# Performance work log

Measured on AMD Instinct MI355X. Metric: run time of the kernel, lower is better.

Reference implementation:

```python
import jax, jax.numpy as jnp
import numpy as np

K_CODES = 512
D_DIM = 64


def setup_inputs() -> dict:
    key = jax.random.key(0)
    k1, k2 = jax.random.split(key)
    # z_e_x: (B, C=D, H, W) encoder output feature map
    z_e_x = jax.random.normal(k1, (32, 64, 64, 64), dtype=jnp.float32)
    # codebook, initialized uniform(-1/K, 1/K) like the torch module
    weight = jax.random.uniform(k2, (K_CODES, D_DIM), dtype=jnp.float32,
                                minval=-1.0 / K_CODES, maxval=1.0 / K_CODES)
    return {"z_e_x": z_e_x, "weight": weight}


def reference(z_e_x, weight):
    # forward(): permute to channels-last, nearest-neighbor codebook lookup,
    # return latent indices of shape (B, H, W)
    z = jnp.transpose(z_e_x, (0, 2, 3, 1))  # (B, H, W, D)
    B, H, W, D = z.shape
    flat = z.reshape(-1, D)  # (N, D)
    # squared L2 distances via expansion: ||z||^2 - 2 z.e + ||e||^2
    dists = (jnp.sum(flat * flat, axis=1, keepdims=True)
             - 2.0 * flat @ weight.T
             + jnp.sum(weight * weight, axis=1))  # (N, K)
    idx = jnp.argmin(dists, axis=1)  # (N,) int
    return idx.reshape(B, H, W)
```

## Files before the change

### kernel.cpp

```cpp
#include <hip/hip_runtime.h>
#include <stdint.h>

#define DCH 64
#define KC 512
#define HWSZ 4096
#define THETA 1e-4f
#define POSB 512
#define BLOCK 1024
#define PADW 65

typedef __attribute__((ext_vector_type(8))) short short8v;
typedef __attribute__((ext_vector_type(4))) float floatx4;

#define WS_WHS   0
#define WS_WLS   65536
#define WS_WNORM 131072
#define WS_CNT   133120
#define WS_LIST  133184
#define WS_NEED  (133184 + 131072 * 4)

__device__ __forceinline__ uint16_t f2bf_rne(float x) {
  uint32_t u = __float_as_uint(x);
  uint32_t r = (u + 0x7fffu + ((u >> 16) & 1u)) >> 16;
  return (uint16_t)r;
}
__device__ __forceinline__ float bf2f(uint16_t b) {
  return __uint_as_float(((uint32_t)b) << 16);
}

__device__ __forceinline__ float pairwise_sq64(const float* __restrict__ a) {
#pragma clang fp contract(off)
  float r0 = a[0]*a[0], r1 = a[1]*a[1], r2 = a[2]*a[2], r3 = a[3]*a[3];
  float r4 = a[4]*a[4], r5 = a[5]*a[5], r6 = a[6]*a[6], r7 = a[7]*a[7];
#pragma unroll
  for (int i = 8; i < 64; i += 8) {
    r0 += a[i+0]*a[i+0]; r1 += a[i+1]*a[i+1];
    r2 += a[i+2]*a[i+2]; r3 += a[i+3]*a[i+3];
    r4 += a[i+4]*a[i+4]; r5 += a[i+5]*a[i+5];
    r6 += a[i+6]*a[i+6]; r7 += a[i+7]*a[i+7];
  }
  return ((r0+r1)+(r2+r3)) + ((r4+r5)+(r6+r7));
}

__device__ __forceinline__ void load_frag(const float* __restrict__ p,
                                          short8v& vh, short8v& vl) {
#pragma unroll
  for (int j = 0; j < 8; ++j) {
    const float v = p[(size_t)j * HWSZ];
    const uint16_t hb = f2bf_rne(v);
    vh[j] = (short)hb;
    vl[j] = (short)f2bf_rne(v - bf2f(hb));
  }
}

__global__ __launch_bounds__(64) void vq_prep(const float* __restrict__ W,
                                              char* __restrict__ ws) {
  const int c = blockIdx.x * 64 + threadIdx.x;
  const float* __restrict__ wr = W + c * DCH;
  float a[64];
#pragma unroll
  for (int i = 0; i < 16; ++i) {
    const float4 v = ((const float4*)wr)[i];
    a[4*i+0] = v.x; a[4*i+1] = v.y; a[4*i+2] = v.z; a[4*i+3] = v.w;
  }
  ((float*)(ws + WS_WNORM))[c] = pairwise_sq64(a);
  uint16_t* wh = (uint16_t*)(ws + WS_WHS);
  uint16_t* wl = (uint16_t*)(ws + WS_WLS);
#pragma unroll
  for (int gd = 0; gd < 8; ++gd) {
    short8v vh, vl;
#pragma unroll
    for (int e = 0; e < 8; ++e) {
      const float v = a[gd * 8 + e];
      const uint16_t hb = f2bf_rne(v);
      vh[e] = (short)hb;
      vl[e] = (short)f2bf_rne(v - bf2f(hb));
    }
    const int go = (gd ^ (c & 7)) << 3;
    *(short8v*)(wh + c * DCH + go) = vh;
    *(short8v*)(wl + c * DCH + go) = vl;
  }
  if (c == 0) *(int*)(ws + WS_CNT) = 0;
}

__global__ __launch_bounds__(BLOCK) void vq_main(const float* __restrict__ Z,
                                                 char* __restrict__ ws,
                                                 int* __restrict__ out) {
  __shared__ uint16_t img[65536];
  __shared__ float wnlds[KC];

  const int tid = threadIdx.x;
  const int lane = tid & 63;
  const int wv = tid >> 6;
  const int csub = lane & 15;
  const int gsub = lane >> 4;
  const int nbase = blockIdx.x * POSB;

  const char* __restrict__ img_src = (const char*)ws;
  const float* __restrict__ wnorm = (const float*)(ws + WS_WNORM);
  int* cnt = (int*)(ws + WS_CNT);
  int* list = (int*)(ws + WS_LIST);

#pragma unroll
  for (int r = 0; r < 8; ++r) {
    const int base = r * 16384 + wv * 1024;
    __builtin_amdgcn_global_load_lds((const uint32_t*)(img_src + base + lane * 16),
                                     (uint32_t*)((char*)img + base), 16, 0, 0);
  }
  if (tid < 128) {
    const int base = wv * 1024;
    __builtin_amdgcn_global_load_lds((const uint32_t*)((const char*)wnorm + base + lane * 16),
                                     (uint32_t*)((char*)wnlds + base), 16, 0, 0);
  }

  short8v ahA0, ahA1, alA0, alA1, ahB0, ahB1, alB0, alB1;
  {
    const int b = nbase >> 12;
    const int hw0 = nbase & 4095;
    const float* zb = Z + (size_t)b * DCH * HWSZ + hw0 + wv * 32 + csub;
    const int dbase = gsub * 8;
    load_frag(zb + (size_t)(dbase +  0) * HWSZ,      ahA0, alA0);
    load_frag(zb + (size_t)(dbase + 32) * HWSZ,      ahA1, alA1);
    load_frag(zb + (size_t)(dbase +  0) * HWSZ + 16, ahB0, alB0);
    load_frag(zb + (size_t)(dbase + 32) * HWSZ + 16, ahB1, alB1);
  }

  float m1A[4], m2A[4], m1B[4], m2B[4];
  int i1A[4], i1B[4];
#pragma unroll
  for (int r = 0; r < 4; ++r) {
    m1A[r] = 3.4e38f; m2A[r] = 3.4e38f; i1A[r] = 0;
    m1B[r] = 3.4e38f; m2B[r] = 3.4e38f; i1B[r] = 0;
  }

  __syncthreads();

  const uint16_t* __restrict__ whl = img;
  const uint16_t* __restrict__ wll = img + 32768;

  const int go0 = (gsub ^ (csub & 7)) << 3;
  const int go1 = ((4 + gsub) ^ (csub & 7)) << 3;

#pragma unroll 8
  for (int kt = 0; kt < KC / 16; ++kt) {
    const int cloc = kt * 16 + csub;
    const float wn = wnlds[cloc];
    const short8v bh0 = *(const short8v*)&whl[cloc * DCH + go0];
    const short8v bh1 = *(const short8v*)&whl[cloc * DCH + go1];
    const short8v bl0 = *(const short8v*)&wll[cloc * DCH + go0];
    const short8v bl1 = *(const short8v*)&wll[cloc * DCH + go1];
    const floatx4 zz = {0.f, 0.f, 0.f, 0.f};
    floatx4 cA1 = __builtin_amdgcn_mfma_f32_16x16x32_bf16(ahA0, bh0, zz, 0, 0, 0);
    floatx4 cB1 = __builtin_amdgcn_mfma_f32_16x16x32_bf16(ahB0, bh0, zz, 0, 0, 0);
    floatx4 cA2 = __builtin_amdgcn_mfma_f32_16x16x32_bf16(ahA0, bl0, zz, 0, 0, 0);
    floatx4 cB2 = __builtin_amdgcn_mfma_f32_16x16x32_bf16(ahB0, bl0, zz, 0, 0, 0);
    floatx4 cA3 = __builtin_amdgcn_mfma_f32_16x16x32_bf16(alA0, bh0, zz, 0, 0, 0);
    floatx4 cB3 = __builtin_amdgcn_mfma_f32_16x16x32_bf16(alB0, bh0, zz, 0, 0, 0);
    cA1 = __builtin_amdgcn_mfma_f32_16x16x32_bf16(ahA1, bh1, cA1, 0, 0, 0);
    cB1 = __builtin_amdgcn_mfma_f32_16x16x32_bf16(ahB1, bh1, cB1, 0, 0, 0);
    cA2 = __builtin_amdgcn_mfma_f32_16x16x32_bf16(ahA1, bl1, cA2, 0, 0, 0);
    cB2 = __builtin_amdgcn_mfma_f32_16x16x32_bf16(ahB1, bl1, cB2, 0, 0, 0);
    cA3 = __builtin_amdgcn_mfma_f32_16x16x32_bf16(alA1, bh1, cA3, 0, 0, 0);
    cB3 = __builtin_amdgcn_mfma_f32_16x16x32_bf16(alB1, bh1, cB3, 0, 0, 0);
#pragma unroll
    for (int r = 0; r < 4; ++r) {
      const float sA = fmaf(-2.0f, (cA1[r] + cA2[r]) + cA3[r], wn);
      i1A[r] = (sA < m1A[r]) ? cloc : i1A[r];
      m2A[r] = fminf(fmaxf(sA, m1A[r]), m2A[r]);
      m1A[r] = fminf(sA, m1A[r]);
      const float sB = fmaf(-2.0f, (cB1[r] + cB2[r]) + cB3[r], wn);
      i1B[r] = (sB < m1B[r]) ? cloc : i1B[r];
      m2B[r] = fminf(fmaxf(sB, m1B[r]), m2B[r]);
      m1B[r] = fminf(sB, m1B[r]);
    }
  }

#pragma unroll
  for (int off = 1; off < 16; off <<= 1) {
#pragma unroll
    for (int r = 0; r < 4; ++r) {
      {
        const float om1 = __shfl_xor(m1A[r], off, 64);
        const float om2 = __shfl_xor(m2A[r], off, 64);
        const int oi = __shfl_xor(i1A[r], off, 64);
        const float nm2 = fminf(fmaxf(m1A[r], om1), fminf(m2A[r], om2));
        i1A[r] = (om1 < m1A[r]) ? oi : i1A[r];
        m1A[r] = fminf(m1A[r], om1);
        m2A[r] = nm2;
      }
      {
        const float om1 = __shfl_xor(m1B[r], off, 64);
        const float om2 = __shfl_xor(m2B[r], off, 64);
        const int oi = __shfl_xor(i1B[r], off, 64);
        const float nm2 = fminf(fmaxf(m1B[r], om1), fminf(m2B[r], om2));
        i1B[r] = (om1 < m1B[r]) ? oi : i1B[r];
        m1B[r] = fminf(m1B[r], om1);
        m2B[r] = nm2;
      }
    }
  }
  if (csub == 0) {
#pragma unroll
    for (int r = 0; r < 4; ++r) {
      const int posA = nbase + wv * 32 + gsub * 4 + r;
      out[posA] = i1A[r];
      if (!(m2A[r] - m1A[r] > THETA)) {
        const int slot = atomicAdd(cnt, 1);
        list[slot] = posA;
      }
      const int posB = posA + 16;
      out[posB] = i1B[r];
      if (!(m2B[r] - m1B[r] > THETA)) {
        const int slot = atomicAdd(cnt, 1);
        list[slot] = posB;
      }
    }
  }
}

__global__ __launch_bounds__(256) void vq_rescue(const float* __restrict__ Z,
                                                 const float* __restrict__ W,
                                                 char* __restrict__ ws,
                                                 int* __restrict__ out) {
  __shared__ float wt[KC * PADW];
  const int cnt = *(const int*)(ws + WS_CNT);
  if (blockIdx.x * 4 >= cnt) return;

  const int lane = threadIdx.x & 63;
  const int wv = threadIdx.x >> 6;
  const int wvg = blockIdx.x * 4 + wv;
  const int* list = (const int*)(ws + WS_LIST);
  const float* wnorm = (const float*)(ws + WS_WNORM);

  for (int c = wv; c < KC; c += 4) {
    wt[c * PADW + lane] = W[c * DCH + lane];
  }
  __syncthreads();

  for (int j = wvg; j < cnt; j += 256 * 4) {
    const int pos = list[j];
    const int b = pos >> 12, hw = pos & 4095;
    float z[DCH];
    const float* zb = Z + ((size_t)b * DCH) * HWSZ + hw;
#pragma unroll
    for (int d = 0; d < DCH; ++d) z[d] = zb[(size_t)d * HWSZ];
    const float znorm = pairwise_sq64(z);
    float bm = 3.4e38f;
    int bi = 0;
#pragma unroll 1
    for (int j2 = 0; j2 < 8; ++j2) {
      const int k = j2 * 64 + lane;
      const float* __restrict__ wrow = &wt[k * PADW];
      float acc = 0.f;
#pragma unroll
      for (int d = 0; d < DCH; ++d) acc = fmaf(z[d], wrow[d], acc);
      const float dist = (znorm - 2.0f * acc) + wnorm[k];
      if (dist < bm) { bm = dist; bi = k; }
    }
#pragma unroll
    for (int off = 32; off >= 1; off >>= 1) {
      const float ov = __shfl_xor(bm, off, 64);
      const int oi = __shfl_xor(bi, off, 64);
      if (ov < bm || (ov == bm && oi < bi)) { bm = ov; bi = oi; }
    }
    if (lane == 0) out[pos] = bi;
  }
}

__global__ __launch_bounds__(256, 4) void vq_fallback(const float* __restrict__ Z,
                                                      const float* __restrict__ W,
                                                      int* __restrict__ out) {
  __shared__ float wnorm[KC];
  __shared__ float cmin[4][64];
  __shared__ int cidx[4][64];
  const int tid = threadIdx.x;
  for (int c = tid; c < KC; c += 256) wnorm[c] = pairwise_sq64(W + c * DCH);
  const int lane = tid & 63;
  const int wv = __builtin_amdgcn_readfirstlane(tid >> 6);
  const int n = blockIdx.x * 64 + lane;
  float z[DCH];
  {
    const int b = n >> 12, hw = n & 4095;
    const float* zbase = Z + ((size_t)b * DCH) * HWSZ + hw;
#pragma unroll
    for (int d = 0; d < DCH; ++d) z[d] = zbase[(size_t)d * HWSZ];
  }
  const float znorm = pairwise_sq64(z);
  __syncthreads();
  float bmin = 3.4e38f;
  int bidx = 0;
  const int k0 = wv * 128;
#pragma unroll 1
  for (int kk = 0; kk < 128; kk += 8) {
    const int k = k0 + kk;
    const float* wr = W + (size_t)k * DCH;
    float acc[8];
#pragma unroll
    for (int j = 0; j < 8; ++j) acc[j] = 0.0f;
#pragma unroll
    for (int d = 0; d < DCH; ++d) {
      const float zd = z[d];
#pragma unroll
      for (int j = 0; j < 8; ++j) acc[j] = fmaf(zd, wr[j * DCH + d], acc[j]);
    }
#pragma unroll
    for (int j = 0; j < 8; ++j) {
      const float dist = (znorm - 2.0f * acc[j]) + wnorm[k + j];
      if (dist < bmin) { bmin = dist; bidx = k + j; }
    }
  }
  cmin[wv][lane] = bmin;
  cidx[wv][lane] = bidx;
  __syncthreads();
  if (tid < 64) {
    float m = cmin[0][tid];
    int ix = cidx[0][tid];
#pragma unroll
    for (int h = 1; h < 4; ++h) {
      if (cmin[h][tid] < m) { m = cmin[h][tid]; ix = cidx[h][tid]; }
    }
    out[blockIdx.x * 64 + tid] = ix;
  }
}

extern "C" void kernel_launch(void* const* d_in, const int* in_sizes, int n_in,
                              void* d_out, int out_size, void* d_ws, size_t ws_size,
                              hipStream_t stream) {
  const float* Z = (const float*)d_in[0];
  const float* W = (const float*)d_in[1];
  int* out = (int*)d_out;
  char* ws = (char*)d_ws;
  const int npos = in_sizes[0] / DCH;

  if (ws_size < (size_t)WS_NEED) {
    vq_fallback<<<npos / 64, 256, 0, stream>>>(Z, W, out);
    return;
  }
  vq_prep<<<8, 64, 0, stream>>>(W, ws);
  vq_main<<<npos / POSB, BLOCK, 0, stream>>>(Z, ws, out);
  vq_rescue<<<256, 256, 0, stream>>>(Z, W, ws, out);
}
```

Measured before the change: 69.71 us.

## Double-buffer codebook staging in LDS and halve positions per block

Each block now handles 256 positions, one 16-row tile per wave instead of two, so the grid has twice as many blocks. The full 128KB codebook image in shared memory is replaced by two 32KB buffers. The codebook is streamed in four quarters, and the next quarter loads while the current one is used by the MFMAs. This cuts the LDS footprint per block, which should allow more blocks per CU and hide the staging latency, at the cost of extra barriers and four times the codebook reloads across the grid.

```diff
diff --git a/kernel.cpp b/kernel.cpp
--- a/kernel.cpp
+++ b/kernel.cpp
@@ -5,7 +5,7 @@
 #define KC 512
 #define HWSZ 4096
 #define THETA 1e-4f
-#define POSB 512
+#define POSB 256
 #define BLOCK 1024
 #define PADW 65
 
@@ -86,7 +86,8 @@
 __global__ __launch_bounds__(BLOCK) void vq_main(const float* __restrict__ Z,
                                                  char* __restrict__ ws,
                                                  int* __restrict__ out) {
-  __shared__ uint16_t img[65536];
+  __shared__ uint16_t buf0[16384];
+  __shared__ uint16_t buf1[16384];
   __shared__ float wnlds[KC];
 
   const int tid = threadIdx.x;
@@ -96,123 +97,100 @@
   const int gsub = lane >> 4;
   const int nbase = blockIdx.x * POSB;
 
-  const char* __restrict__ img_src = (const char*)ws;
+  const char* __restrict__ src_hi = (const char*)ws;
+  const char* __restrict__ src_lo = (const char*)ws + WS_WLS;
   const float* __restrict__ wnorm = (const float*)(ws + WS_WNORM);
   int* cnt = (int*)(ws + WS_CNT);
   int* list = (int*)(ws + WS_LIST);
 
-#pragma unroll
-  for (int r = 0; r < 8; ++r) {
-    const int base = r * 16384 + wv * 1024;
-    __builtin_amdgcn_global_load_lds((const uint32_t*)(img_src + base + lane * 16),
-                                     (uint32_t*)((char*)img + base), 16, 0, 0);
-  }
+  auto STAGE = [&](int q, uint16_t* dst) {
+    const int off = tid * 16;
+    __builtin_amdgcn_global_load_lds((const uint32_t*)(src_hi + q * 16384 + off),
+                                     (uint32_t*)((char*)dst + off), 16, 0, 0);
+    __builtin_amdgcn_global_load_lds((const uint32_t*)(src_lo + q * 16384 + off),
+                                     (uint32_t*)((char*)dst + 16384 + off), 16, 0, 0);
+  };
+
+  STAGE(0, buf0);
   if (tid < 128) {
     const int base = wv * 1024;
     __builtin_amdgcn_global_load_lds((const uint32_t*)((const char*)wnorm + base + lane * 16),
                                      (uint32_t*)((char*)wnlds + base), 16, 0, 0);
   }
 
-  short8v ahA0, ahA1, alA0, alA1, ahB0, ahB1, alB0, alB1;
+  short8v ah0, ah1, al0, al1;
   {
     const int b = nbase >> 12;
     const int hw0 = nbase & 4095;
-    const float* zb = Z + (size_t)b * DCH * HWSZ + hw0 + wv * 32 + csub;
+    const float* zb = Z + (size_t)b * DCH * HWSZ + hw0 + wv * 16 + csub;
     const int dbase = gsub * 8;
-    load_frag(zb + (size_t)(dbase +  0) * HWSZ,      ahA0, alA0);
-    load_frag(zb + (size_t)(dbase + 32) * HWSZ,      ahA1, alA1);
-    load_frag(zb + (size_t)(dbase +  0) * HWSZ + 16, ahB0, alB0);
-    load_frag(zb + (size_t)(dbase + 32) * HWSZ + 16, ahB1, alB1);
-  }
-
-  float m1A[4], m2A[4], m1B[4], m2B[4];
-  int i1A[4], i1B[4];
-#pragma unroll
-  for (int r = 0; r < 4; ++r) {
-    m1A[r] = 3.4e38f; m2A[r] = 3.4e38f; i1A[r] = 0;
-    m1B[r] = 3.4e38f; m2B[r] = 3.4e38f; i1B[r] = 0;
-  }
+    load_frag(zb + (size_t)(dbase +  0) * HWSZ, ah0, al0);
+    load_frag(zb + (size_t)(dbase + 32) * HWSZ, ah1, al1);
+  }
+
+  float m1[4], m2[4];
+  int i1[4];
+#pragma unroll
+  for (int r = 0; r < 4; ++r) { m1[r] = 3.4e38f; m2[r] = 3.4e38f; i1[r] = 0; }
 
   __syncthreads();
-
-  const uint16_t* __restrict__ whl = img;
-  const uint16_t* __restrict__ wll = img + 32768;
 
   const int go0 = (gsub ^ (csub & 7)) << 3;
   const int go1 = ((4 + gsub) ^ (csub & 7)) << 3;
 
-#pragma unroll 8
-  for (int kt = 0; kt < KC / 16; ++kt) {
-    const int cloc = kt * 16 + csub;
-    const float wn = wnlds[cloc];
-    const short8v bh0 = *(const short8v*)&whl[cloc * DCH + go0];
-    const short8v bh1 = *(const short8v*)&whl[cloc * DCH + go1];
-    const short8v bl0 = *(const short8v*)&wll[cloc * DCH + go0];
-    const short8v bl1 = *(const short8v*)&wll[cloc * DCH + go1];
-    const floatx4 zz = {0.f, 0.f, 0.f, 0.f};
-    floatx4 cA1 = __builtin_amdgcn_mfma_f32_16x16x32_bf16(ahA0, bh0, zz, 0, 0, 0);
-    floatx4 cB1 = __builtin_amdgcn_mfma_f32_16x16x32_bf16(ahB0, bh0, zz, 0, 0, 0);
-    floatx4 cA2 = __builtin_amdgcn_mfma_f32_16x16x32_bf16(ahA0, bl0, zz, 0, 0, 0);
-    floatx4 cB2 = __builtin_amdgcn_mfma_f32_16x16x32_bf16(ahB0, bl0, zz, 0, 0, 0);
-    floatx4 cA3 = __builtin_amdgcn_mfma_f32_16x16x32_bf16(alA0, bh0, zz, 0, 0, 0);
-    floatx4 cB3 = __builtin_amdgcn_mfma_f32_16x16x32_bf16(alB0, bh0, zz, 0, 0, 0);
-    cA1 = __builtin_amdgcn_mfma_f32_16x16x32_bf16(ahA1, bh1, cA1, 0, 0, 0);
-    cB1 = __builtin_amdgcn_mfma_f32_16x16x32_bf16(ahB1, bh1, cB1, 0, 0, 0);
-    cA2 = __builtin_amdgcn_mfma_f32_16x16x32_bf16(ahA1, bl1, cA2, 0, 0, 0);
-    cB2 = __builtin_amdgcn_mfma_f32_16x16x32_bf16(ahB1, bl1, cB2, 0, 0, 0);
-    cA3 = __builtin_amdgcn_mfma_f32_16x16x32_bf16(alA1, bh1, cA3, 0, 0, 0);
-    cB3 = __builtin_amdgcn_mfma_f32_16x16x32_bf16(alB1, bh1, cB3, 0, 0, 0);
+#pragma unroll
+  for (int q = 0; q < 4; ++q) {
+    if (q < 3) STAGE(q + 1, (q & 1) ? buf0 : buf1);
+    const uint16_t* __restrict__ bh = (q & 1) ? buf1 : buf0;
+    const uint16_t* __restrict__ bl = bh + 8192;
+#pragma unroll
+    for (int kt = 0; kt < 8; ++kt) {
+      const int cq = kt * 16 + csub;
+      const int cloc = q * 128 + cq;
+      const float wn = wnlds[cloc];
+      const short8v bh0 = *(const short8v*)&bh[cq * DCH + go0];
+      const short8v bh1 = *(const short8v*)&bh[cq * DCH + go1];
+      const short8v bl0 = *(const short8v*)&bl[cq * DCH + go0];
+      const short8v bl1 = *(const short8v*)&bl[cq * DCH + go1];
+      const floatx4 zz = {0.f, 0.f, 0.f, 0.f};
+      floatx4 c1 = __builtin_amdgcn_mfma_f32_16x16x32_bf16(ah0, bh0, zz, 0, 0, 0);
+      floatx4 c2 = __builtin_amdgcn_mfma_f32_16x16x32_bf16(ah0, bl0, zz, 0, 0, 0);
+      floatx4 c3 = __builtin_amdgcn_mfma_f32_16x16x32_bf16(al0, bh0, zz, 0, 0, 0);
+      c1 = __builtin_amdgcn_mfma_f32_16x16x32_bf16(ah1, bh1, c1, 0, 0, 0);
+      c2 = __builtin_amdgcn_mfma_f32_16x16x32_bf16(ah1, bl1, c2, 0, 0, 0);
+      c3 = __builtin_amdgcn_mfma_f32_16x16x32_bf16(al1, bh1, c3, 0, 0, 0);
+#pragma unroll
+      for (int r = 0; r < 4; ++r) {
+        const float s = fmaf(-2.0f, (c1[r] + c2[r]) + c3[r], wn);
+        i1[r] = (s < m1[r]) ? cloc : i1[r];
+        m2[r] = fminf(fmaxf(s, m1[r]), m2[r]);
+        m1[r] = fminf(s, m1[r]);
+      }
+    }
+    if (q < 3) __syncthreads();
+  }
+
+#pragma unroll
+  for (int off = 1; off < 16; off <<= 1) {
 #pragma unroll
     for (int r = 0; r < 4; ++r) {
-      const float sA = fmaf(-2.0f, (cA1[r] + cA2[r]) + cA3[r], wn);
-      i1A[r] = (sA < m1A[r]) ? cloc : i1A[r];
-      m2A[r] = fminf(fmaxf(sA, m1A[r]), m2A[r]);
-      m1A[r] = fminf(sA, m1A[r]);
-      const float sB = fmaf(-2.0f, (cB1[r] + cB2[r]) + cB3[r], wn);
-      i1B[r] = (sB < m1B[r]) ? cloc : i1B[r];
-      m2B[r] = fminf(fmaxf(sB, m1B[r]), m2B[r]);
-      m1B[r] = fminf(sB, m1B[r]);
-    }
-  }
-
-#pragma unroll
-  for (int off = 1; off < 16; off <<= 1) {
+      const float om1 = __shfl_xor(m1[r], off, 64);
+      const float om2 = __shfl_xor(m2[r], off, 64);
+      const int oi = __shfl_xor(i1[r], off, 64);
+      const float nm2 = fminf(fmaxf(m1[r], om1), fminf(m2[r], om2));
+      i1[r] = (om1 < m1[r]) ? oi : i1[r];
+      m1[r] = fminf(m1[r], om1);
+      m2[r] = nm2;
+    }
+  }
+  if (csub == 0) {
 #pragma unroll
     for (int r = 0; r < 4; ++r) {
-      {
-        const float om1 = __shfl_xor(m1A[r], off, 64);
-        const float om2 = __shfl_xor(m2A[r], off, 64);
-        const int oi = __shfl_xor(i1A[r], off, 64);
-        const float nm2 = fminf(fmaxf(m1A[r], om1), fminf(m2A[r], om2));
-        i1A[r] = (om1 < m1A[r]) ? oi : i1A[r];
-        m1A[r] = fminf(m1A[r], om1);
-        m2A[r] = nm2;
-      }
-      {
-        const float om1 = __shfl_xor(m1B[r], off, 64);
-        const float om2 = __shfl_xor(m2B[r], off, 64);
-        const int oi = __shfl_xor(i1B[r], off, 64);
-        const float nm2 = fminf(fmaxf(m1B[r], om1), fminf(m2B[r], om2));
-        i1B[r] = (om1 < m1B[r]) ? oi : i1B[r];
-        m1B[r] = fminf(m1B[r], om1);
-        m2B[r] = nm2;
-      }
-    }
-  }
-  if (csub == 0) {
-#pragma unroll
-    for (int r = 0; r < 4; ++r) {
-      const int posA = nbase + wv * 32 + gsub * 4 + r;
-      out[posA] = i1A[r];
-      if (!(m2A[r] - m1A[r] > THETA)) {
+      const int pos = nbase + wv * 16 + gsub * 4 + r;
+      out[pos] = i1[r];
+      if (!(m2[r] - m1[r] > THETA)) {
         const int slot = atomicAdd(cnt, 1);
-        list[slot] = posA;
-      }
-      const int posB = posA + 16;
-      out[posB] = i1B[r];
-      if (!(m2B[r] - m1B[r] > THETA)) {
-        const int slot = atomicAdd(cnt, 1);
-        list[slot] = posB;
+        list[slot] = pos;
       }
     }
   }
```

New measurement: 85.90 us. 23.2% more time.

## Split codebook across two blocks per position tile and merge partial argmins

Applied to the files above, without the earlier changes.

The main kernel now processes half the codebook (256 codes) per block, launching twice as many blocks, each staging only half the bf16 hi/lo codebook image in LDS. Per-position partial min, second-min and index are written to workspace, and a new combine kernel merges the halves, writes the output and queues ambiguous positions for the existing rescue pass. The intent is more blocks and lower LDS use per block, so occupancy and wave-level parallelism improve on a grid that previously had only 256 blocks. The cost is an extra launch, the Z fragments being loaded and converted twice, and extra global traffic for the partial results. The workspace must also be large enough for the new path to run.

```diff
diff --git a/kernel.cpp b/kernel.cpp
--- a/kernel.cpp
+++ b/kernel.cpp
@@ -3,10 +3,12 @@
 
 #define DCH 64
 #define KC 512
+#define KHALF 256
 #define HWSZ 4096
 #define THETA 1e-4f
 #define POSB 512
 #define BLOCK 1024
+#define NPOS 131072
 #define PADW 65
 
 typedef __attribute__((ext_vector_type(8))) short short8v;
@@ -18,6 +20,10 @@
 #define WS_CNT   133120
 #define WS_LIST  133184
 #define WS_NEED  (133184 + 131072 * 4)
+#define WS_PM1   657472
+#define WS_PM2   (657472 + 1048576)
+#define WS_PI    (657472 + 2097152)
+#define WS_NEED_SPLIT (657472 + 3145728)
 
 __device__ __forceinline__ uint16_t f2bf_rne(float x) {
   uint32_t u = __float_as_uint(x);
@@ -83,34 +89,35 @@
   if (c == 0) *(int*)(ws + WS_CNT) = 0;
 }
 
-__global__ __launch_bounds__(BLOCK) void vq_main(const float* __restrict__ Z,
-                                                 char* __restrict__ ws,
-                                                 int* __restrict__ out) {
-  __shared__ uint16_t img[65536];
-  __shared__ float wnlds[KC];
+__global__ __launch_bounds__(BLOCK) void vq_main_split(const float* __restrict__ Z,
+                                                       char* __restrict__ ws,
+                                                       int npos) {
+  __shared__ uint16_t img[32768];
+  __shared__ float wnlds[KHALF];
 
   const int tid = threadIdx.x;
   const int lane = tid & 63;
   const int wv = tid >> 6;
   const int csub = lane & 15;
   const int gsub = lane >> 4;
-  const int nbase = blockIdx.x * POSB;
-
-  const char* __restrict__ img_src = (const char*)ws;
+  const int h = blockIdx.x & 1;
+  const int nbase = (blockIdx.x >> 1) * POSB;
+
+  const char* __restrict__ src_hi = (const char*)ws + (size_t)h * 32768;
+  const char* __restrict__ src_lo = (const char*)ws + WS_WLS + (size_t)h * 32768;
   const float* __restrict__ wnorm = (const float*)(ws + WS_WNORM);
-  int* cnt = (int*)(ws + WS_CNT);
-  int* list = (int*)(ws + WS_LIST);
-
-#pragma unroll
-  for (int r = 0; r < 8; ++r) {
+
+#pragma unroll
+  for (int r = 0; r < 2; ++r) {
     const int base = r * 16384 + wv * 1024;
-    __builtin_amdgcn_global_load_lds((const uint32_t*)(img_src + base + lane * 16),
+    __builtin_amdgcn_global_load_lds((const uint32_t*)(src_hi + base + lane * 16),
                                      (uint32_t*)((char*)img + base), 16, 0, 0);
-  }
-  if (tid < 128) {
-    const int base = wv * 1024;
-    __builtin_amdgcn_global_load_lds((const uint32_t*)((const char*)wnorm + base + lane * 16),
-                                     (uint32_t*)((char*)wnlds + base), 16, 0, 0);
+    __builtin_amdgcn_global_load_lds((const uint32_t*)(src_lo + base + lane * 16),
+                                     (uint32_t*)((char*)img + 32768 + base), 16, 0, 0);
+  }
+  if (tid < 64) {
+    __builtin_amdgcn_global_load_lds((const uint32_t*)((const char*)wnorm + h * 1024 + lane * 16),
+                                     (uint32_t*)((char*)wnlds), 16, 0, 0);
   }
 
   short8v ahA0, ahA1, alA0, alA1, ahB0, ahB1, alB0, alB1;
@@ -136,8 +143,162 @@
   __syncthreads();
 
   const uint16_t* __restrict__ whl = img;
+  const uint16_t* __restrict__ wll = img + 16384;
+
+  const int go0 = (gsub ^ (csub & 7)) << 3;
+  const int go1 = ((4 + gsub) ^ (csub & 7)) << 3;
+
+#pragma unroll 8
+  for (int kt = 0; kt < KHALF / 16; ++kt) {
+    const int cq = kt * 16 + csub;
+    const int cloc = h * KHALF + cq;
+    const float wn = wnlds[cq];
+    const short8v bh0 = *(const short8v*)&whl[cq * DCH + go0];
+    const short8v bh1 = *(const short8v*)&whl[cq * DCH + go1];
+    const short8v bl0 = *(const short8v*)&wll[cq * DCH + go0];
+    const short8v bl1 = *(const short8v*)&wll[cq * DCH + go1];
+    const floatx4 zz = {0.f, 0.f, 0.f, 0.f};
+    floatx4 cA1 = __builtin_amdgcn_mfma_f32_16x16x32_bf16(ahA0, bh0, zz, 0, 0, 0);
+    floatx4 cB1 = __builtin_amdgcn_mfma_f32_16x16x32_bf16(ahB0, bh0, zz, 0, 0, 0);
+    floatx4 cA2 = __builtin_amdgcn_mfma_f32_16x16x32_bf16(ahA0, bl0, zz, 0, 0, 0);
+    floatx4 cB2 = __builtin_amdgcn_mfma_f32_16x16x32_bf16(ahB0, bl0, zz, 0, 0, 0);
+    floatx4 cA3 = __builtin_amdgcn_mfma_f32_16x16x32_bf16(alA0, bh0, zz, 0, 0, 0);
+    floatx4 cB3 = __builtin_amdgcn_mfma_f32_16x16x32_bf16(alB0, bh0, zz, 0, 0, 0);
+    cA1 = __builtin_amdgcn_mfma_f32_16x16x32_bf16(ahA1, bh1, cA1, 0, 0, 0);
+    cB1 = __builtin_amdgcn_mfma_f32_16x16x32_bf16(ahB1, bh1, cB1, 0, 0, 0);
+    cA2 = __builtin_amdgcn_mfma_f32_16x16x32_bf16(ahA1, bl1, cA2, 0, 0, 0);
+    cB2 = __builtin_amdgcn_mfma_f32_16x16x32_bf16(ahB1, bl1, cB2, 0, 0, 0);
+    cA3 = __builtin_amdgcn_mfma_f32_16x16x32_bf16(alA1, bh1, cA3, 0, 0, 0);
+    cB3 = __builtin_amdgcn_mfma_f32_16x16x32_bf16(alB1, bh1, cB3, 0, 0, 0);
+#pragma unroll
+    for (int r = 0; r < 4; ++r) {
+      const float sA = fmaf(-2.0f, (cA1[r] + cA2[r]) + cA3[r], wn);
+      i1A[r] = (sA < m1A[r]) ? cloc : i1A[r];
+      m2A[r] = fminf(fmaxf(sA, m1A[r]), m2A[r]);
+      m1A[r] = fminf(sA, m1A[r]);
+      const float sB = fmaf(-2.0f, (cB1[r] + cB2[r]) + cB3[r], wn);
+      i1B[r] = (sB < m1B[r]) ? cloc : i1B[r];
+      m2B[r] = fminf(fmaxf(sB, m1B[r]), m2B[r]);
+      m1B[r] = fminf(sB, m1B[r]);
+    }
+  }
+
+#pragma unroll
+  for (int off = 1; off < 16; off <<= 1) {
+#pragma unroll
+    for (int r = 0; r < 4; ++r) {
+      {
+        const float om1 = __shfl_xor(m1A[r], off, 64);
+        const float om2 = __shfl_xor(m2A[r], off, 64);
+        const int oi = __shfl_xor(i1A[r], off, 64);
+        const float nm2 = fminf(fmaxf(m1A[r], om1), fminf(m2A[r], om2));
+        i1A[r] = (om1 < m1A[r]) ? oi : i1A[r];
+        m1A[r] = fminf(m1A[r], om1);
+        m2A[r] = nm2;
+      }
+      {
+        const float om1 = __shfl_xor(m1B[r], off, 64);
+        const float om2 = __shfl_xor(m2B[r], off, 64);
+        const int oi = __shfl_xor(i1B[r], off, 64);
+        const float nm2 = fminf(fmaxf(m1B[r], om1), fminf(m2B[r], om2));
+        i1B[r] = (om1 < m1B[r]) ? oi : i1B[r];
+        m1B[r] = fminf(m1B[r], om1);
+        m2B[r] = nm2;
+      }
+    }
+  }
+  if (csub == 0) {
+    float* pm1 = (float*)(ws + WS_PM1) + (size_t)h * npos;
+    float* pm2 = (float*)(ws + WS_PM2) + (size_t)h * npos;
+    int* pi = (int*)(ws + WS_PI) + (size_t)h * npos;
+#pragma unroll
+    for (int r = 0; r < 4; ++r) {
+      const int posA = nbase + wv * 32 + gsub * 4 + r;
+      pm1[posA] = m1A[r]; pm2[posA] = m2A[r]; pi[posA] = i1A[r];
+      const int posB = posA + 16;
+      pm1[posB] = m1B[r]; pm2[posB] = m2B[r]; pi[posB] = i1B[r];
+    }
+  }
+}
+
+__global__ __launch_bounds__(256) void vq_combine(char* __restrict__ ws,
+                                                  int* __restrict__ out,
+                                                  int npos) {
+  const int pos = blockIdx.x * 256 + threadIdx.x;
+  if (pos >= npos) return;
+  const float* pm1 = (const float*)(ws + WS_PM1);
+  const float* pm2 = (const float*)(ws + WS_PM2);
+  const int* pi = (const int*)(ws + WS_PI);
+  int* cnt = (int*)(ws + WS_CNT);
+  int* list = (int*)(ws + WS_LIST);
+
+  const float m1a = pm1[pos], m1b = pm1[npos + pos];
+  const float m2a = pm2[pos], m2b = pm2[npos + pos];
+  const int ia = pi[pos], ib = pi[npos + pos];
+  const int idx = (m1b < m1a) ? ib : ia;
+  const float m1 = fminf(m1a, m1b);
+  const float m2 = fminf(fmaxf(m1a, m1b), fminf(m2a, m2b));
+  out[pos] = idx;
+  if (!(m2 - m1 > THETA)) {
+    const int slot = atomicAdd(cnt, 1);
+    list[slot] = pos;
+  }
+}
+
+__global__ __launch_bounds__(BLOCK) void vq_main_full(const float* __restrict__ Z,
+                                                      char* __restrict__ ws,
+                                                      int* __restrict__ out) {
+  __shared__ uint16_t img[65536];
+  __shared__ float wnlds[KC];
+
+  const int tid = threadIdx.x;
+  const int lane = tid & 63;
+  const int wv = tid >> 6;
+  const int csub = lane & 15;
+  const int gsub = lane >> 4;
+  const int nbase = blockIdx.x * POSB;
+
+  const char* __restrict__ img_src = (const char*)ws;
+  const float* __restrict__ wnorm = (const float*)(ws + WS_WNORM);
+  int* cnt = (int*)(ws + WS_CNT);
+  int* list = (int*)(ws + WS_LIST);
+
+#pragma unroll
+  for (int r = 0; r < 8; ++r) {
+    const int base = r * 16384 + wv * 1024;
+    __builtin_amdgcn_global_load_lds((const uint32_t*)(img_src + base + lane * 16),
+                                     (uint32_t*)((char*)img + base), 16, 0, 0);
+  }
+  if (tid < 128) {
+    const int base = wv * 1024;
+    __builtin_amdgcn_global_load_lds((const uint32_t*)((const char*)wnorm + base + lane * 16),
+                                     (uint32_t*)((char*)wnlds + base), 16, 0, 0);
+  }
+
+  short8v ahA0, ahA1, alA0, alA1, ahB0, ahB1, alB0, alB1;
+  {
+    const int b = nbase >> 12;
+    const int hw0 = nbase & 4095;
+    const float* zb = Z + (size_t)b * DCH * HWSZ + hw0 + wv * 32 + csub;
+    const int dbase = gsub * 8;
+    load_frag(zb + (size_t)(dbase +  0) * HWSZ,      ahA0, alA0);
+    load_frag(zb + (size_t)(dbase + 32) * HWSZ,      ahA1, alA1);
+    load_frag(zb + (size_t)(dbase +  0) * HWSZ + 16, ahB0, alB0);
+    load_frag(zb + (size_t)(dbase + 32) * HWSZ + 16, ahB1, alB1);
+  }
+
+  float m1A[4], m2A[4], m1B[4], m2B[4];
+  int i1A[4], i1B[4];
+#pragma unroll
+  for (int r = 0; r < 4; ++r) {
+    m1A[r] = 3.4e38f; m2A[r] = 3.4e38f; i1A[r] = 0;
+    m1B[r] = 3.4e38f; m2B[r] = 3.4e38f; i1B[r] = 0;
+  }
+
+  __syncthreads();
+
+  const uint16_t* __restrict__ whl = img;
   const uint16_t* __restrict__ wll = img + 32768;
-
   const int go0 = (gsub ^ (csub & 7)) << 3;
   const int go1 = ((4 + gsub) ^ (csub & 7)) << 3;
 
@@ -332,11 +493,16 @@
   char* ws = (char*)d_ws;
   const int npos = in_sizes[0] / DCH;
 
-  if (ws_size < (size_t)WS_NEED) {
+  if (ws_size >= (size_t)WS_NEED_SPLIT) {
+    vq_prep<<<8, 64, 0, stream>>>(W, ws);
+    vq_main_split<<<(npos / POSB) * 2, BLOCK, 0, stream>>>(Z, ws, npos);
+    vq_combine<<<(npos + 255) / 256, 256, 0, stream>>>(ws, out, npos);
+    vq_rescue<<<256, 256, 0, stream>>>(Z, W, ws, out);
+  } else if (ws_size >= (size_t)WS_NEED) {
+    vq_prep<<<8, 64, 0, stream>>>(W, ws);
+    vq_main_full<<<npos / POSB, BLOCK, 0, stream>>>(Z, ws, out);
+    vq_rescue<<<256, 256, 0, stream>>>(Z, W, ws, out);
+  } else {
     vq_fallback<<<npos / 64, 256, 0, stream>>>(Z, W, out);
-    return;
-  }
-  vq_prep<<<8, 64, 0, stream>>>(W, ws);
-  vq_main<<<npos / POSB, BLOCK, 0, stream>>>(Z, ws, out);
-  vq_rescue<<<256, 256, 0, stream>>>(Z, W, ws, out);
-}
+  }
+}
```

After: 86.78 us. 24.5% more time.
